# Kernel optimization log

Hardware: AMD Instinct MI355X
Metric: run time of the kernel (lower is better)

Reference implementation:

```python
import jax, jax.numpy as jnp
import numpy as np
import math

D_MODEL = 512
NUM_HEADS = 8
HEAD_DIM = D_MODEL // NUM_HEADS
B, L = 2, 2048
LN_EPS = 1e-5
DEN_EPS = 1e-5


def setup_inputs() -> dict:
    key = jax.random.key(0)
    ks = jax.random.split(key, 6)
    s = 1.0 / math.sqrt(D_MODEL)
    return {
        "x": jax.random.normal(ks[0], (B, L, D_MODEL), dtype=jnp.float32),
        "Wqkv": jax.random.normal(ks[1], (D_MODEL, 3 * D_MODEL), dtype=jnp.float32) * s,
        "bqkv": jnp.zeros((3 * D_MODEL,), dtype=jnp.float32),
        "Wout": jax.random.normal(ks[2], (D_MODEL, D_MODEL), dtype=jnp.float32) * s,
        "bout": jnp.zeros((D_MODEL,), dtype=jnp.float32),
        "ln_gamma": jnp.ones((D_MODEL,), dtype=jnp.float32),
        "ln_beta": jnp.zeros((D_MODEL,), dtype=jnp.float32),
        "decay_logits": jnp.full((NUM_HEADS,), 5.0, dtype=jnp.float32),
    }


def reference(x, Wqkv, bqkv, Wout, bout, ln_gamma, ln_beta, decay_logits):
    Bv, Lv, D = x.shape
    H = decay_logits.shape[0]
    E = D // H

    qkv = x @ Wqkv + bqkv                                   # [B,L,3D]
    q, k, v = jnp.split(qkv, 3, axis=-1)
    q = q.reshape(Bv, Lv, H, E)
    k = k.reshape(Bv, Lv, H, E)
    v = v.reshape(Bv, Lv, H, E)

    # ELU feature map + 1 -> positive features; scale q by 1/sqrt(E)
    q = (jax.nn.elu(q) + 1.0) / jnp.sqrt(jnp.asarray(E, x.dtype))
    k = jax.nn.elu(k) + 1.0

    lambdas = jax.nn.sigmoid(decay_logits).reshape(1, 1, H, 1)   # [1,1,H,1]
    t = jnp.arange(Lv, dtype=x.dtype).reshape(1, Lv, 1, 1)       # [1,L,1,1]
    decay_k = jnp.power(lambdas, -t)   # lambda^{-t}
    decay_q = jnp.power(lambdas, t)    # lambda^{t}

    k_dec = k * decay_k                                          # [B,L,H,E]
    kv = jnp.einsum('blhe,blhf->blhef', k_dec, v)                # [B,L,H,E,E]
    memory = jnp.cumsum(kv, axis=1)                              # prefix-sum scan over L
    k_sum = jnp.cumsum(k_dec, axis=1)                            # [B,L,H,E]

    q_dec = q * decay_q
    num = jnp.einsum('blhe,blhef->blhf', q_dec, memory)          # [B,L,H,E]
    den = jnp.einsum('blhe,blhe->blh', q_dec, k_sum)[..., None] + DEN_EPS
    out = (num / den).reshape(Bv, Lv, D)

    out = out @ Wout + bout

    # LayerNorm (eval mode; dropout is identity)
    mu = jnp.mean(out, axis=-1, keepdims=True)
    var = jnp.var(out, axis=-1, keepdims=True)
    out = (out - mu) / jnp.sqrt(var + LN_EPS) * ln_gamma + ln_beta
    return out
```

## Files before the change

kernel.cpp:

```cpp
#include <hip/hip_runtime.h>
#include <math.h>

#define B_ 2
#define L_ 2048
#define D_ 512
#define H_ 8
#define E_ 64
#define CHUNK 32
#define NCH 64
#define DEN_EPS_ 1e-5f
#define LN_EPS_ 1e-5f

typedef __bf16 bf16x8 __attribute__((ext_vector_type(8)));
typedef __bf16 bf16x4 __attribute__((ext_vector_type(4)));
typedef float  f32x4  __attribute__((ext_vector_type(4)));

__device__ __forceinline__ float sigm(float x) { return 1.f / (1.f + expf(-x)); }
__device__ __forceinline__ float elu1(float x) { return x > 0.f ? x + 1.f : expf(x); }

__device__ __forceinline__ void async_cp16(const void* g, void* l) {
    __builtin_amdgcn_global_load_lds(
        (const __attribute__((address_space(1))) void*)g,
        (__attribute__((address_space(3))) void*)l, 16, 0, 0);
}

#define SWZ4(row, q) ((((q) ^ ((row) & 3)) * 8))

__global__ __launch_bounds__(256) void k_prep(
    const float* __restrict__ W1, __bf16* __restrict__ D1,
    const float* __restrict__ W2, __bf16* __restrict__ D2,
    const float* __restrict__ X,  __bf16* __restrict__ Xb)
{
    const int t = threadIdx.x;
    if (blockIdx.z == 2) {
        int id = ((int)blockIdx.y * 32 + (int)blockIdx.x) * 256 + t;
#pragma unroll
        for (int it = 0; it < 4; it++) {
            size_t i = (size_t)it * 524288 + (size_t)id * 8;
            float4 a = *(const float4*)&X[i];
            float4 b = *(const float4*)&X[i + 4];
            bf16x8 o;
            o[0] = (__bf16)a.x; o[1] = (__bf16)a.y; o[2] = (__bf16)a.z; o[3] = (__bf16)a.w;
            o[4] = (__bf16)b.x; o[5] = (__bf16)b.y; o[6] = (__bf16)b.z; o[7] = (__bf16)b.w;
            *(bf16x8*)&Xb[i] = o;
        }
        return;
    }
    const float* src; __bf16* dst; int N;
    if (blockIdx.z == 0) { if (blockIdx.x >= 24) return; src = W1; dst = D1; N = 1536; }
    else                 { if (blockIdx.x >= 8)  return; src = W2; dst = D2; N = 512; }
    const int K = 512;

    __shared__ __bf16 tile[64][68];
    const int kb = blockIdx.y * 64, nb = blockIdx.x * 64;
    const int rr = t >> 4, cc4 = (t & 15) * 4;
#pragma unroll
    for (int p = 0; p < 4; p++) {
        int k = rr + p * 16;
        float4 v = *(const float4*)&src[(size_t)(kb + k) * N + nb + cc4];
        tile[k][cc4 + 0] = (__bf16)v.x;
        tile[k][cc4 + 1] = (__bf16)v.y;
        tile[k][cc4 + 2] = (__bf16)v.z;
        tile[k][cc4 + 3] = (__bf16)v.w;
    }
    __syncthreads();
#pragma unroll
    for (int p = 0; p < 4; p++) {
        int n = rr + p * 16;
        bf16x4 o;
        o[0] = tile[cc4 + 0][n];
        o[1] = tile[cc4 + 1][n];
        o[2] = tile[cc4 + 2][n];
        o[3] = tile[cc4 + 3][n];
        *(bf16x4*)&dst[(size_t)(nb + n) * K + kb + cc4] = o;
    }
}

__global__ __launch_bounds__(256) void k_mfma_qkv(
    const __bf16* __restrict__ Ab, const __bf16* __restrict__ Bt,
    const float* __restrict__ bias,
    __bf16* __restrict__ Qb, __bf16* __restrict__ Kb, __bf16* __restrict__ Vb)
{
    __shared__ __bf16 Al[64 * 32];
    __shared__ __bf16 Bl[128 * 32];
    const int t = threadIdx.x;
    const int w = t >> 6, lane = t & 63;
    const int wm = w >> 1, wn = w & 1;
    const int ll = lane & 15, quad = lane >> 4;
    const int m0 = blockIdx.y * 64, n0 = blockIdx.x * 128;

    f32x4 acc[2][4] = {};
    const int sr  = t >> 2;
    const int skz = (((t & 3) ^ (sr & 3)) * 8);

    __bf16* A0  = &Al[(w * 16) * 32];
    __bf16* B0  = &Bl[(w * 16) * 32];
    __bf16* B1p = &Bl[(64 + w * 16) * 32];

    for (int k0 = 0; k0 < D_; k0 += 32) {
        async_cp16(&Ab[(size_t)(m0 + sr) * D_ + k0 + skz],      A0);
        async_cp16(&Bt[(size_t)(n0 + sr) * D_ + k0 + skz],      B0);
        async_cp16(&Bt[(size_t)(n0 + 64 + sr) * D_ + k0 + skz], B1p);
        __syncthreads();
#pragma unroll
        for (int im = 0; im < 2; im++) {
            int ra = wm * 32 + im * 16 + ll;
            bf16x8 a = *(const bf16x8*)&Al[ra * 32 + SWZ4(ra, quad)];
#pragma unroll
            for (int in = 0; in < 4; in++) {
                int rb = wn * 64 + in * 16 + ll;
                bf16x8 b = *(const bf16x8*)&Bl[rb * 32 + SWZ4(rb, quad)];
                acc[im][in] = __builtin_amdgcn_mfma_f32_16x16x32_bf16(a, b, acc[im][in], 0, 0, 0);
            }
        }
        __syncthreads();
    }

    const int sec = n0 >> 9;
    __bf16* base = (sec == 0 ? Qb : (sec == 1 ? Kb : Vb));
#pragma unroll
    for (int im = 0; im < 2; im++) {
#pragma unroll
        for (int in = 0; in < 4; in++) {
            int n = n0 + wn * 64 + in * 16 + ll;
            int d = n & 511, h = d >> 6, e = d & 63;
            float bv = bias[n];
#pragma unroll
            for (int r = 0; r < 4; r++) {
                int m = m0 + wm * 32 + im * 16 + quad * 4 + r;
                int bb = m >> 11, l = m & 2047;
                float v = acc[im][in][r] + bv;
                if (sec == 0)      v = elu1(v) * 0.125f;
                else if (sec == 1) v = elu1(v);
                base[((size_t)((bb * H_ + h) * L_ + l)) * E_ + e] = (__bf16)v;
            }
        }
    }
}

__global__ __launch_bounds__(256) void k_chunk_g(
    const __bf16* __restrict__ Kb, const __bf16* __restrict__ Vb,
    const float* __restrict__ dl,
    __bf16* __restrict__ Gt, float* __restrict__ gn)
{
    __shared__ __bf16 Kwt[64][40];
    __shared__ __bf16 Vt[64][40];
    const int t  = threadIdx.x;
    const int bx = blockIdx.x;
    const int n = bx & 63, h = (bx >> 6) & 7, bb = bx >> 9;
    const int bh = bb * H_ + h;
    const float lam = sigm(dl[h]);

    {
        int i = t & 31, e0 = (t >> 5) * 8;
        size_t src = ((size_t)bh * L_ + n * CHUNK + i) * E_ + e0;
        float wk = powf(lam, (float)(CHUNK - 1 - i));
        bf16x8 k8 = *(const bf16x8*)&Kb[src];
        bf16x8 v8 = *(const bf16x8*)&Vb[src];
#pragma unroll
        for (int q = 0; q < 8; q++) {
            Kwt[e0 + q][i] = (__bf16)((float)k8[q] * wk);
            Vt[e0 + q][i]  = v8[q];
        }
    }
    __syncthreads();

    const int w = t >> 6, lane = t & 63;
    const int wm = w >> 1, wn = w & 1;
    const int ll = lane & 15, quad = lane >> 4;

    bf16x8 af[2], bf_[2];
#pragma unroll
    for (int a = 0; a < 2; a++) {
        af[a]  = *(const bf16x8*)&Vt[wm * 32 + a * 16 + ll][quad * 8];
        bf_[a] = *(const bf16x8*)&Kwt[wn * 32 + a * 16 + ll][quad * 8];
    }
    f32x4 acc[2][2] = {};
#pragma unroll
    for (int a = 0; a < 2; a++)
#pragma unroll
        for (int b = 0; b < 2; b++)
            acc[a][b] = __builtin_amdgcn_mfma_f32_16x16x32_bf16(af[a], bf_[b], acc[a][b], 0, 0, 0);

    size_t gbase = ((size_t)bh * NCH + n) * 4096;
#pragma unroll
    for (int a = 0; a < 2; a++)
#pragma unroll
        for (int b = 0; b < 2; b++)
#pragma unroll
            for (int r = 0; r < 4; r++) {
                int f = wm * 32 + a * 16 + quad * 4 + r;
                int e = wn * 32 + b * 16 + ll;
                Gt[gbase + (size_t)f * 64 + e] = (__bf16)acc[a][b][r];
            }

    if (t < 64) {
        float ga = 0.f;
#pragma unroll
        for (int k8 = 0; k8 < 4; k8++) {
            bf16x8 kk = *(const bf16x8*)&Kwt[t][k8 * 8];
#pragma unroll
            for (int q = 0; q < 8; q++) ga += (float)kk[q];
        }
        gn[((size_t)bh * NCH + n) * E_ + t] = ga;
    }
}

__global__ __launch_bounds__(64) void k_scan_par(
    const __bf16* __restrict__ Gt, const float* __restrict__ gn,
    const float* __restrict__ dl,
    __bf16* __restrict__ Sb, float* __restrict__ zl)
{
    const int lane = threadIdx.x;
    const int bh = blockIdx.x >> 6;
    const int j  = blockIdx.x & 63;
    const float lam = sigm(dl[bh & 7]);
    const float dC  = powf(lam, (float)CHUNK);

    const size_t base = ((size_t)bh * NCH) * 4096 + (size_t)j * 64 + lane;

    __bf16 g[NCH];
#pragma unroll
    for (int n = 0; n < NCH; n++) g[n] = Gt[base + (size_t)n * 4096];

    float s = 0.f;
#pragma unroll
    for (int n = 0; n < NCH; n++) {
        Sb[base + (size_t)n * 4096] = (__bf16)(lam * s);
        s = fmaf(dC, s, (float)g[n]);
    }

    float gv = gn[((size_t)bh * NCH + lane) * E_ + j];
    float wf = dC;
#pragma unroll
    for (int k = 1; k < 64; k <<= 1) {
        float up = __shfl_up(gv, k);
        if (lane >= k) gv = fmaf(wf, up, gv);
        wf = wf * wf;
    }
    float zex = __shfl_up(gv, 1);
    if (lane == 0) zex = 0.f;
    zl[((size_t)bh * NCH + lane) * E_ + j] = lam * zex;
}

__global__ __launch_bounds__(256) void k_attn(
    const __bf16* __restrict__ Qb, const __bf16* __restrict__ Kb,
    const __bf16* __restrict__ Vb,
    const __bf16* __restrict__ Sb, const float* __restrict__ zl,
    const float* __restrict__ dl, __bf16* __restrict__ Out)
{
    __shared__ __bf16 Qw[32][64];
    __shared__ __bf16 Kw[32][64];
    __shared__ __bf16 Vt[64][40];
    __shared__ __bf16 A1[32][40];
    __shared__ float  den[32];
    __shared__ float  zz[64];

    const int t  = threadIdx.x;
    const int bx = blockIdx.x;
    const int n = bx & 63, h = (bx >> 6) & 7, bb = bx >> 9;
    const int bh = bb * H_ + h;
    const float lam = sigm(dl[h]);

    const int w = t >> 6, lane = t & 63;
    const int ll = lane & 15, quad = lane >> 4;
    const int fw = w * 16;
    const size_t sbase = ((size_t)bh * NCH + n) * 4096;

    bf16x8 bS0 = *(const bf16x8*)&Sb[sbase + (size_t)(fw + ll) * 64 + quad * 8];
    bf16x8 bS1 = *(const bf16x8*)&Sb[sbase + (size_t)(fw + ll) * 64 + 32 + quad * 8];

    {
        int i = t >> 3, e0c = t & 7;
        size_t src = ((size_t)bh * L_ + n * CHUNK + i) * E_ + e0c * 8;
        float wq = powf(lam, (float)i);
        float wk = powf(lam, -(float)i);
        bf16x8 q8 = *(const bf16x8*)&Qb[src];
        bf16x8 k8 = *(const bf16x8*)&Kb[src];
        bf16x8 v8 = *(const bf16x8*)&Vb[src];
        bf16x8 qo, ko;
        int e0 = e0c * 8;
#pragma unroll
        for (int q = 0; q < 8; q++) {
            qo[q] = (__bf16)((float)q8[q] * wq);
            ko[q] = (__bf16)((float)k8[q] * wk);
            Vt[e0 + q][i] = v8[q];
        }
        int cs = (e0c ^ (i & 7)) * 8;
        *(bf16x8*)&Qw[i][cs] = qo;
        *(bf16x8*)&Kw[i][cs] = ko;
        if (t < 64) zz[t] = zl[((size_t)bh * NCH + n) * E_ + t];
    }
    __syncthreads();

    {
        const int wm = w >> 1, wn = w & 1;
        int ra = wm * 16 + ll, rb = wn * 16 + ll;
        f32x4 accA = {};
#pragma unroll
        for (int ks = 0; ks < 2; ks++) {
            bf16x8 a = *(const bf16x8*)&Qw[ra][((ks * 4 + quad) ^ (ra & 7)) * 8];
            bf16x8 b = *(const bf16x8*)&Kw[rb][((ks * 4 + quad) ^ (rb & 7)) * 8];
            accA = __builtin_amdgcn_mfma_f32_16x16x32_bf16(a, b, accA, 0, 0, 0);
        }
        int j = wn * 16 + ll;
#pragma unroll
        for (int r = 0; r < 4; r++) {
            int i = wm * 16 + quad * 4 + r;
            A1[i][j] = (__bf16)(j <= i ? accA[r] : 0.f);
        }
    }
    __syncthreads();

    if (t < 32) {
        float rs = 0.f;
#pragma unroll
        for (int k8 = 0; k8 < 4; k8++) {
            bf16x8 aa = *(const bf16x8*)&A1[t][k8 * 8];
#pragma unroll
            for (int q = 0; q < 8; q++) rs += (float)aa[q];
        }
        float qz = 0.f;
#pragma unroll
        for (int e8 = 0; e8 < 8; e8++) {
            bf16x8 qq = *(const bf16x8*)&Qw[t][(e8 ^ (t & 7)) * 8];
#pragma unroll
            for (int q = 0; q < 8; q++) qz += (float)qq[q] * zz[e8 * 8 + q];
        }
        den[t] = rs + qz + DEN_EPS_;
    }

    f32x4 acc1[2] = {}, acc2[2] = {};
    {
        bf16x8 bV = *(const bf16x8*)&Vt[fw + ll][quad * 8];
#pragma unroll
        for (int im = 0; im < 2; im++) {
            bf16x8 aA = *(const bf16x8*)&A1[im * 16 + ll][quad * 8];
            acc1[im] = __builtin_amdgcn_mfma_f32_16x16x32_bf16(aA, bV, acc1[im], 0, 0, 0);
        }
#pragma unroll
        for (int im = 0; im < 2; im++) {
            int ra = im * 16 + ll;
            bf16x8 aQ0 = *(const bf16x8*)&Qw[ra][((quad) ^ (ra & 7)) * 8];
            bf16x8 aQ1 = *(const bf16x8*)&Qw[ra][((4 + quad) ^ (ra & 7)) * 8];
            acc2[im] = __builtin_amdgcn_mfma_f32_16x16x32_bf16(aQ0, bS0, acc2[im], 0, 0, 0);
            acc2[im] = __builtin_amdgcn_mfma_f32_16x16x32_bf16(aQ1, bS1, acc2[im], 0, 0, 0);
        }
    }
    __syncthreads();

#pragma unroll
    for (int im = 0; im < 2; im++)
#pragma unroll
        for (int r = 0; r < 4; r++) {
            int i = im * 16 + quad * 4 + r;
            float o = (acc1[im][r] + acc2[im][r]) / den[i];
            Out[((size_t)bb * L_ + n * CHUNK + i) * D_ + h * E_ + fw + ll] = (__bf16)o;
        }
}

__global__ __launch_bounds__(256) void k_mfma_out_ln(
    const __bf16* __restrict__ Ab, const __bf16* __restrict__ Bt,
    const float* __restrict__ bias, const float* __restrict__ gam,
    const float* __restrict__ bet, float* __restrict__ Y)
{
    __shared__ __bf16 Al[16 * 32];
    __shared__ __bf16 Bl[512 * 32];
    __shared__ float gaml[512], betl[512], bl[512];
    __shared__ float redS[4][16], redQ[4][16];
    __shared__ float mv[16][2];

    const int t = threadIdx.x;
    const int w = t >> 6, lane = t & 63;
    const int ll = lane & 15, quad = lane >> 4;
    const int m0 = blockIdx.x * 16;

    {
        float2 g = *(const float2*)&gam[t * 2];
        float2 b2 = *(const float2*)&bet[t * 2];
        float2 bo = *(const float2*)&bias[t * 2];
        gaml[t * 2] = g.x;  gaml[t * 2 + 1] = g.y;
        betl[t * 2] = b2.x; betl[t * 2 + 1] = b2.y;
        bl[t * 2]   = bo.x; bl[t * 2 + 1]   = bo.y;
    }

    f32x4 acc[8] = {};
    const int sr  = t >> 2;
    const int skz = (((t & 3) ^ (sr & 3)) * 8);

    for (int k0 = 0; k0 < D_; k0 += 32) {
        if (t < 64)
            async_cp16(&Ab[(size_t)(m0 + sr) * D_ + k0 + skz], &Al[0]);
#pragma unroll
        for (int p = 0; p < 8; p++)
            async_cp16(&Bt[(size_t)(p * 64 + sr) * D_ + k0 + skz], &Bl[(p * 64 + w * 16) * 32]);
        __syncthreads();
        bf16x8 a = *(const bf16x8*)&Al[ll * 32 + SWZ4(ll, quad)];
#pragma unroll
        for (int in = 0; in < 8; in++) {
            int rb = w * 128 + in * 16 + ll;
            bf16x8 b = *(const bf16x8*)&Bl[rb * 32 + SWZ4(rb, quad)];
            acc[in] = __builtin_amdgcn_mfma_f32_16x16x32_bf16(a, b, acc[in], 0, 0, 0);
        }
        __syncthreads();
    }

    float vals[8][4];
    float ps[4] = {}, pq[4] = {};
#pragma unroll
    for (int in = 0; in < 8; in++) {
        int col = w * 128 + in * 16 + ll;
        float bv = bl[col];
#pragma unroll
        for (int r = 0; r < 4; r++) {
            float v = acc[in][r] + bv;
            vals[in][r] = v;
            ps[r] += v;
            pq[r] += v * v;
        }
    }
#pragma unroll
    for (int r = 0; r < 4; r++) {
        float s = ps[r], q = pq[r];
        s += __shfl_xor(s, 1); q += __shfl_xor(q, 1);
        s += __shfl_xor(s, 2); q += __shfl_xor(q, 2);
        s += __shfl_xor(s, 4); q += __shfl_xor(q, 4);
        s += __shfl_xor(s, 8); q += __shfl_xor(q, 8);
        if (ll == 0) {
            int row = quad * 4 + r;
            redS[w][row] = s;
            redQ[w][row] = q;
        }
    }
    __syncthreads();
    if (t < 16) {
        float S = redS[0][t] + redS[1][t] + redS[2][t] + redS[3][t];
        float Q = redQ[0][t] + redQ[1][t] + redQ[2][t] + redQ[3][t];
        float mu  = S * (1.f / 512.f);
        float var = Q * (1.f / 512.f) - mu * mu;
        mv[t][0] = mu;
        mv[t][1] = rsqrtf(var + LN_EPS_);
    }
    __syncthreads();
#pragma unroll
    for (int r = 0; r < 4; r++) {
        int row = quad * 4 + r;
        float mu = mv[row][0], rs = mv[row][1];
#pragma unroll
        for (int in = 0; in < 8; in++) {
            int col = w * 128 + in * 16 + ll;
            Y[(size_t)(m0 + row) * D_ + col] =
                (vals[in][r] - mu) * rs * gaml[col] + betl[col];
        }
    }
}

extern "C" void kernel_launch(void* const* d_in, const int* in_sizes, int n_in,
                              void* d_out, int out_size, void* d_ws, size_t ws_size,
                              hipStream_t stream)
{
    const float* x    = (const float*)d_in[0];
    const float* Wqkv = (const float*)d_in[1];
    const float* bqkv = (const float*)d_in[2];
    const float* Wout = (const float*)d_in[3];
    const float* bout = (const float*)d_in[4];
    const float* gam  = (const float*)d_in[5];
    const float* bet  = (const float*)d_in[6];
    const float* dl   = (const float*)d_in[7];
    float* out = (float*)d_out;

    const size_t NBHLE = (size_t)B_ * H_ * L_ * E_;
    const size_t NG    = (size_t)B_ * H_ * NCH * E_ * E_;
    const size_t Ng    = (size_t)B_ * H_ * NCH * E_;

    char* p = (char*)d_ws;
    __bf16* Gt  = (__bf16*)p;    p += NG * 2;
    __bf16* Sb  = (__bf16*)p;    p += NG * 2;
    float*  gn  = (float*)p;     p += Ng * 4;
    float*  zl  = (float*)p;     p += Ng * 4;
    __bf16* Qb  = (__bf16*)p;    p += NBHLE * 2;
    __bf16* Kb  = (__bf16*)p;    p += NBHLE * 2;
    __bf16* Vb  = (__bf16*)p;    p += NBHLE * 2;
    __bf16* Xb    = (__bf16*)p;  p += NBHLE * 2;
    __bf16* WqkvT = (__bf16*)p;  p += (size_t)1536 * 512 * 2;
    __bf16* WoutT = (__bf16*)p;  p += (size_t)512 * 512 * 2;
    __bf16* Ao    = (__bf16*)p;  p += NBHLE * 2;

    dim3 blk(256);
    k_prep        <<<dim3(32, 8, 3), blk, 0, stream>>>(Wqkv, WqkvT, Wout, WoutT, x, Xb);
    k_mfma_qkv    <<<dim3(12, 64),   blk, 0, stream>>>(Xb, WqkvT, bqkv, Qb, Kb, Vb);
    k_chunk_g     <<<dim3(1024),     blk, 0, stream>>>(Kb, Vb, dl, Gt, gn);
    k_scan_par    <<<dim3(1024),     dim3(64), 0, stream>>>(Gt, gn, dl, Sb, zl);
    k_attn        <<<dim3(1024),     blk, 0, stream>>>(Qb, Kb, Vb, Sb, zl, dl, Ao);
    k_mfma_out_ln <<<dim3(256),      blk, 0, stream>>>(Ao, WoutT, bout, gam, bet, out);
}
```

Baseline: 128.1 us.

## Fuse x conversion into QKV GEMM, double-buffer GEMMs, stage epilogue stores

Drops the separate fp32-to-bf16 pass over x. The QKV GEMM now loads fp32 x directly, converts it in registers and writes it to LDS. Both GEMMs double-buffer their K-loop tiles, so the next tile's loads overlap the current MFMAs, and the QKV epilogue is staged through LDS so each thread writes two 16-byte vectors to the head-major layout. Separately, powf is replaced with exp2f/log2f for the decay weights. The extra LDS (about 66KB in the out-LN kernel) may lower occupancy, and the x reads are now synchronous global loads that are not swizzled in the same way as before.

```diff
diff --git a/kernel.cpp b/kernel.cpp
--- a/kernel.cpp
+++ b/kernel.cpp
@@ -26,33 +26,19 @@
 
 #define SWZ4(row, q) ((((q) ^ ((row) & 3)) * 8))
 
-__global__ __launch_bounds__(256) void k_prep(
+__global__ __launch_bounds__(256) void k_prep_w(
     const float* __restrict__ W1, __bf16* __restrict__ D1,
-    const float* __restrict__ W2, __bf16* __restrict__ D2,
-    const float* __restrict__ X,  __bf16* __restrict__ Xb)
+    const float* __restrict__ W2, __bf16* __restrict__ D2)
 {
     const int t = threadIdx.x;
-    if (blockIdx.z == 2) {
-        int id = ((int)blockIdx.y * 32 + (int)blockIdx.x) * 256 + t;
-#pragma unroll
-        for (int it = 0; it < 4; it++) {
-            size_t i = (size_t)it * 524288 + (size_t)id * 8;
-            float4 a = *(const float4*)&X[i];
-            float4 b = *(const float4*)&X[i + 4];
-            bf16x8 o;
-            o[0] = (__bf16)a.x; o[1] = (__bf16)a.y; o[2] = (__bf16)a.z; o[3] = (__bf16)a.w;
-            o[4] = (__bf16)b.x; o[5] = (__bf16)b.y; o[6] = (__bf16)b.z; o[7] = (__bf16)b.w;
-            *(bf16x8*)&Xb[i] = o;
-        }
-        return;
-    }
-    const float* src; __bf16* dst; int N;
-    if (blockIdx.z == 0) { if (blockIdx.x >= 24) return; src = W1; dst = D1; N = 1536; }
-    else                 { if (blockIdx.x >= 8)  return; src = W2; dst = D2; N = 512; }
+    const int bx = blockIdx.x;
+    const float* src; __bf16* dst; int N, xt;
+    if (bx < 24) { src = W1; dst = D1; N = 1536; xt = bx; }
+    else         { src = W2; dst = D2; N = 512;  xt = bx - 24; }
     const int K = 512;
 
     __shared__ __bf16 tile[64][68];
-    const int kb = blockIdx.y * 64, nb = blockIdx.x * 64;
+    const int kb = blockIdx.y * 64, nb = xt * 64;
     const int rr = t >> 4, cc4 = (t & 15) * 4;
 #pragma unroll
     for (int p = 0; p < 4; p++) {
@@ -77,12 +63,11 @@
 }
 
 __global__ __launch_bounds__(256) void k_mfma_qkv(
-    const __bf16* __restrict__ Ab, const __bf16* __restrict__ Bt,
+    const float* __restrict__ X, const __bf16* __restrict__ Bt,
     const float* __restrict__ bias,
     __bf16* __restrict__ Qb, __bf16* __restrict__ Kb, __bf16* __restrict__ Vb)
 {
-    __shared__ __bf16 Al[64 * 32];
-    __shared__ __bf16 Bl[128 * 32];
+    __shared__ __bf16 lds[12288];
     const int t = threadIdx.x;
     const int w = t >> 6, lane = t & 63;
     const int wm = w >> 1, wn = w & 1;
@@ -90,51 +75,91 @@
     const int m0 = blockIdx.y * 64, n0 = blockIdx.x * 128;
 
     f32x4 acc[2][4] = {};
-    const int sr  = t >> 2;
-    const int skz = (((t & 3) ^ (sr & 3)) * 8);
-
-    __bf16* A0  = &Al[(w * 16) * 32];
-    __bf16* B0  = &Bl[(w * 16) * 32];
-    __bf16* B1p = &Bl[(64 + w * 16) * 32];
+    const int sr = t >> 2;
+    const int c4 = t & 3;
+    const int gA = (c4 ^ (sr & 3));
+    const int skz = gA * 8;
+
+    float4 pa0, pa1;
+    auto fetchA = [&](int k0) {
+        const float* ap = X + (size_t)(m0 + sr) * D_ + k0 + skz;
+        pa0 = *(const float4*)ap;
+        pa1 = *(const float4*)(ap + 4);
+    };
+    auto issueB = [&](int k0, int nbuf) {
+        __bf16* b0 = &lds[4096 + nbuf * 4096 + (w * 16) * 32];
+        __bf16* b1 = &lds[4096 + nbuf * 4096 + (64 + w * 16) * 32];
+        async_cp16(&Bt[(size_t)(n0 + sr) * D_ + k0 + skz],      b0);
+        async_cp16(&Bt[(size_t)(n0 + 64 + sr) * D_ + k0 + skz], b1);
+    };
+    auto writeA = [&](int nbuf) {
+        bf16x8 o;
+        o[0] = (__bf16)pa0.x; o[1] = (__bf16)pa0.y;
+        o[2] = (__bf16)pa0.z; o[3] = (__bf16)pa0.w;
+        o[4] = (__bf16)pa1.x; o[5] = (__bf16)pa1.y;
+        o[6] = (__bf16)pa1.z; o[7] = (__bf16)pa1.w;
+        *(bf16x8*)&lds[nbuf * 2048 + sr * 32 + c4 * 8] = o;
+    };
+
+    fetchA(0);
+    issueB(0, 0);
+    writeA(0);
+    __syncthreads();
 
     for (int k0 = 0; k0 < D_; k0 += 32) {
-        async_cp16(&Ab[(size_t)(m0 + sr) * D_ + k0 + skz],      A0);
-        async_cp16(&Bt[(size_t)(n0 + sr) * D_ + k0 + skz],      B0);
-        async_cp16(&Bt[(size_t)(n0 + 64 + sr) * D_ + k0 + skz], B1p);
-        __syncthreads();
+        const int buf = (k0 >> 5) & 1, nbuf = buf ^ 1;
+        const int nk = k0 + 32;
+        if (nk < D_) { fetchA(nk); issueB(nk, nbuf); }
+        const int ao = buf * 2048, bo = 4096 + buf * 4096;
 #pragma unroll
         for (int im = 0; im < 2; im++) {
             int ra = wm * 32 + im * 16 + ll;
-            bf16x8 a = *(const bf16x8*)&Al[ra * 32 + SWZ4(ra, quad)];
+            bf16x8 a = *(const bf16x8*)&lds[ao + ra * 32 + SWZ4(ra, quad)];
 #pragma unroll
             for (int in = 0; in < 4; in++) {
                 int rb = wn * 64 + in * 16 + ll;
-                bf16x8 b = *(const bf16x8*)&Bl[rb * 32 + SWZ4(rb, quad)];
+                bf16x8 b = *(const bf16x8*)&lds[bo + rb * 32 + SWZ4(rb, quad)];
                 acc[im][in] = __builtin_amdgcn_mfma_f32_16x16x32_bf16(a, b, acc[im][in], 0, 0, 0);
             }
         }
+        if (nk < D_) writeA(nbuf);
         __syncthreads();
     }
 
     const int sec = n0 >> 9;
-    __bf16* base = (sec == 0 ? Qb : (sec == 1 ? Kb : Vb));
 #pragma unroll
     for (int im = 0; im < 2; im++) {
 #pragma unroll
         for (int in = 0; in < 4; in++) {
-            int n = n0 + wn * 64 + in * 16 + ll;
-            int d = n & 511, h = d >> 6, e = d & 63;
-            float bv = bias[n];
+            int nc = wn * 64 + in * 16 + ll;
+            float bv = bias[n0 + nc];
 #pragma unroll
             for (int r = 0; r < 4; r++) {
-                int m = m0 + wm * 32 + im * 16 + quad * 4 + r;
-                int bb = m >> 11, l = m & 2047;
+                int mr = wm * 32 + im * 16 + quad * 4 + r;
                 float v = acc[im][in][r] + bv;
                 if (sec == 0)      v = elu1(v) * 0.125f;
                 else if (sec == 1) v = elu1(v);
-                base[((size_t)((bb * H_ + h) * L_ + l)) * E_ + e] = (__bf16)v;
+                lds[mr * 132 + nc] = (__bf16)v;
             }
         }
+    }
+    __syncthreads();
+
+    __bf16* base = (sec == 0 ? Qb : (sec == 1 ? Kb : Vb));
+    const int hbase = (n0 & 511) >> 6;
+#pragma unroll
+    for (int u = 0; u < 2; u++) {
+        int id = u * 256 + t;
+        int row = id >> 3;
+        int c0  = (id & 7) * 16;
+        bf16x8 v0 = *(bf16x8*)&lds[row * 132 + c0];
+        bf16x8 v1 = *(bf16x8*)&lds[row * 132 + c0 + 8];
+        int h = hbase + (c0 >> 6);
+        int e0 = c0 & 63;
+        int m = m0 + row, bb2 = m >> 11, l = m & 2047;
+        __bf16* dst = base + ((size_t)((bb2 * H_ + h) * L_ + l)) * E_ + e0;
+        *(bf16x8*)dst       = v0;
+        *(bf16x8*)(dst + 8) = v1;
     }
 }
 
@@ -150,11 +175,12 @@
     const int n = bx & 63, h = (bx >> 6) & 7, bb = bx >> 9;
     const int bh = bb * H_ + h;
     const float lam = sigm(dl[h]);
+    const float l2  = log2f(lam);
 
     {
         int i = t & 31, e0 = (t >> 5) * 8;
         size_t src = ((size_t)bh * L_ + n * CHUNK + i) * E_ + e0;
-        float wk = powf(lam, (float)(CHUNK - 1 - i));
+        float wk = exp2f(l2 * (float)(CHUNK - 1 - i));
         bf16x8 k8 = *(const bf16x8*)&Kb[src];
         bf16x8 v8 = *(const bf16x8*)&Vb[src];
 #pragma unroll
@@ -215,7 +241,7 @@
     const int bh = blockIdx.x >> 6;
     const int j  = blockIdx.x & 63;
     const float lam = sigm(dl[bh & 7]);
-    const float dC  = powf(lam, (float)CHUNK);
+    const float dC  = exp2f(32.f * log2f(lam));
 
     const size_t base = ((size_t)bh * NCH) * 4096 + (size_t)j * 64 + lane;
 
@@ -261,6 +287,7 @@
     const int n = bx & 63, h = (bx >> 6) & 7, bb = bx >> 9;
     const int bh = bb * H_ + h;
     const float lam = sigm(dl[h]);
+    const float l2  = log2f(lam);
 
     const int w = t >> 6, lane = t & 63;
     const int ll = lane & 15, quad = lane >> 4;
@@ -273,8 +300,8 @@
     {
         int i = t >> 3, e0c = t & 7;
         size_t src = ((size_t)bh * L_ + n * CHUNK + i) * E_ + e0c * 8;
-        float wq = powf(lam, (float)i);
-        float wk = powf(lam, -(float)i);
+        float wq = exp2f(l2 * (float)i);
+        float wk = exp2f(-l2 * (float)i);
         bf16x8 q8 = *(const bf16x8*)&Qb[src];
         bf16x8 k8 = *(const bf16x8*)&Kb[src];
         bf16x8 v8 = *(const bf16x8*)&Vb[src];
@@ -364,8 +391,7 @@
     const float* __restrict__ bias, const float* __restrict__ gam,
     const float* __restrict__ bet, float* __restrict__ Y)
 {
-    __shared__ __bf16 Al[16 * 32];
-    __shared__ __bf16 Bl[512 * 32];
+    __shared__ __bf16 lds[33792];
     __shared__ float gaml[512], betl[512], bl[512];
     __shared__ float redS[4][16], redQ[4][16];
     __shared__ float mv[16][2];
@@ -388,18 +414,28 @@
     const int sr  = t >> 2;
     const int skz = (((t & 3) ^ (sr & 3)) * 8);
 
+    auto issue = [&](int k0, int buf) {
+        if (t < 64)
+            async_cp16(&Ab[(size_t)(m0 + sr) * D_ + k0 + skz], &lds[buf * 512]);
+#pragma unroll
+        for (int p = 0; p < 8; p++)
+            async_cp16(&Bt[(size_t)(p * 64 + sr) * D_ + k0 + skz],
+                       &lds[1024 + buf * 16384 + (p * 64 + w * 16) * 32]);
+    };
+
+    issue(0, 0);
+    __syncthreads();
+
     for (int k0 = 0; k0 < D_; k0 += 32) {
-        if (t < 64)
-            async_cp16(&Ab[(size_t)(m0 + sr) * D_ + k0 + skz], &Al[0]);
-#pragma unroll
-        for (int p = 0; p < 8; p++)
-            async_cp16(&Bt[(size_t)(p * 64 + sr) * D_ + k0 + skz], &Bl[(p * 64 + w * 16) * 32]);
-        __syncthreads();
-        bf16x8 a = *(const bf16x8*)&Al[ll * 32 + SWZ4(ll, quad)];
+        const int buf = (k0 >> 5) & 1, nbuf = buf ^ 1;
+        const int nk = k0 + 32;
+        if (nk < D_) issue(nk, nbuf);
+        const int ao = buf * 512, bo = 1024 + buf * 16384;
+        bf16x8 a = *(const bf16x8*)&lds[ao + ll * 32 + SWZ4(ll, quad)];
 #pragma unroll
         for (int in = 0; in < 8; in++) {
             int rb = w * 128 + in * 16 + ll;
-            bf16x8 b = *(const bf16x8*)&Bl[rb * 32 + SWZ4(rb, quad)];
+            bf16x8 b = *(const bf16x8*)&lds[bo + rb * 32 + SWZ4(rb, quad)];
             acc[in] = __builtin_amdgcn_mfma_f32_16x16x32_bf16(a, b, acc[in], 0, 0, 0);
         }
         __syncthreads();
@@ -481,16 +517,15 @@
     __bf16* Qb  = (__bf16*)p;    p += NBHLE * 2;
     __bf16* Kb  = (__bf16*)p;    p += NBHLE * 2;
     __bf16* Vb  = (__bf16*)p;    p += NBHLE * 2;
-    __bf16* Xb    = (__bf16*)p;  p += NBHLE * 2;
     __bf16* WqkvT = (__bf16*)p;  p += (size_t)1536 * 512 * 2;
     __bf16* WoutT = (__bf16*)p;  p += (size_t)512 * 512 * 2;
     __bf16* Ao    = (__bf16*)p;  p += NBHLE * 2;
 
     dim3 blk(256);
-    k_prep        <<<dim3(32, 8, 3), blk, 0, stream>>>(Wqkv, WqkvT, Wout, WoutT, x, Xb);
-    k_mfma_qkv    <<<dim3(12, 64),   blk, 0, stream>>>(Xb, WqkvT, bqkv, Qb, Kb, Vb);
-    k_chunk_g     <<<dim3(1024),     blk, 0, stream>>>(Kb, Vb, dl, Gt, gn);
-    k_scan_par    <<<dim3(1024),     dim3(64), 0, stream>>>(Gt, gn, dl, Sb, zl);
-    k_attn        <<<dim3(1024),     blk, 0, stream>>>(Qb, Kb, Vb, Sb, zl, dl, Ao);
-    k_mfma_out_ln <<<dim3(256),      blk, 0, stream>>>(Ao, WoutT, bout, gam, bet, out);
-}
+    k_prep_w      <<<dim3(32, 8),  blk, 0, stream>>>(Wqkv, WqkvT, Wout, WoutT);
+    k_mfma_qkv    <<<dim3(12, 64), blk, 0, stream>>>(x, WqkvT, bqkv, Qb, Kb, Vb);
+    k_chunk_g     <<<dim3(1024),   blk, 0, stream>>>(Kb, Vb, dl, Gt, gn);
+    k_scan_par    <<<dim3(1024),   dim3(64), 0, stream>>>(Gt, gn, dl, Sb, zl);
+    k_attn        <<<dim3(1024),   blk, 0, stream>>>(Qb, Kb, Vb, Sb, zl, dl, Ao);
+    k_mfma_out_ln <<<dim3(256),    blk, 0, stream>>>(Ao, WoutT, bout, gam, bet, out);
+}
```

Measured after the change: 128.6 us. About the same (+0.4%).
